# Kernel tuning notes

Measured on AMD Instinct MI355X. Metric: run time of the kernel, lower is better.

## Reference

```python
import jax, jax.numpy as jnp
from jax import lax
import numpy as np

H = 2048
LX = 32
LY = 32


def setup_inputs() -> dict:
    key = jax.random.key(0)
    ks = jax.random.split(key, 9)
    N = LX * LY
    s = 1.0 / np.sqrt(H).astype(np.float32)
    inp = {
        "x": jax.random.normal(ks[0], (N,), jnp.float32),
        # embed: Dense(1 -> H)
        "We": jax.random.normal(ks[1], (1, H), jnp.float32),
        "be": jnp.zeros((H,), jnp.float32),
        # GRUCell input gates (with bias)
        "Wir": jax.random.normal(ks[2], (H, H), jnp.float32) * s,
        "bir": jnp.zeros((H,), jnp.float32),
        "Wiz": jax.random.normal(ks[3], (H, H), jnp.float32) * s,
        "biz": jnp.zeros((H,), jnp.float32),
        "Win": jax.random.normal(ks[4], (H, H), jnp.float32) * s,
        "bin_": jnp.zeros((H,), jnp.float32),
        # GRUCell recurrent gates (hr/hz bias-free, hn with bias, as in flax)
        "Whr": jax.random.normal(ks[5], (H, H), jnp.float32) * s,
        "Whz": jax.random.normal(ks[6], (H, H), jnp.float32) * s,
        "Whn": jax.random.normal(ks[7], (H, H), jnp.float32) * s,
        "bhn": jnp.zeros((H,), jnp.float32),
        "Lx": LX,
        "Ly": LY,
    }
    return inp


def snake_order(Lx: int, Ly: int):
    idx = np.arange(Lx * Ly).reshape(Ly, Lx)
    idx[1::2] = idx[1::2, ::-1]  # reverse odd rows -> snake pattern
    return jnp.asarray(idx.reshape(-1))


def reference(x, We, be, Wir, bir, Wiz, biz, Win, bin_, Whr, Whz, Whn, bhn, Lx, Ly):
    order = snake_order(Lx, Ly)                      # (N,) visit order
    # embed each scalar site value: Dense(1->H), vectorized over all sites
    xe = x[order][:, None] * We[0][None, :] + be     # (N, H)
    # precompute input-gate projections for all steps (same math, batched)
    a_r = xe @ Wir + bir                             # (N, H)
    a_z = xe @ Wiz + biz
    a_n = xe @ Win + bin_
    h0 = jnp.zeros((Whr.shape[0],), xe.dtype)

    def step(h, g):
        ar, az, an = g
        r = jax.nn.sigmoid(ar + h @ Whr)
        z = jax.nn.sigmoid(az + h @ Whz)
        n = jnp.tanh(an + r * (h @ Whn + bhn))
        h_new = (1.0 - z) * n + z * h
        return h_new, None

    h, _ = lax.scan(step, h0, (a_r, a_z, a_n))
    return h
```

## Files before the change

### kernel.cpp

```cpp
#include <hip/hip_runtime.h>

#define HDIM 2048
#define TSTEPS 1024
#define NBLK 256
#define NTHR 512
#define CPB 8
#define TAGM 0x3FFu
#define NREP 8
#define RSTRIDE 2112u
#define SPIN_CAP (1 << 21)

typedef unsigned long long ull;

__device__ __forceinline__ int snake_src(int t) {
    int y = t >> 5, p = t & 31;
    return (y & 1) ? (y * 32 + 31 - p) : t;
}
__device__ __forceinline__ float sigmoid_f(float v) {
    return __builtin_amdgcn_rcpf(1.f + __expf(-v));
}
__device__ __forceinline__ float tanh_f(float v) {
    return 1.f - 2.f * __builtin_amdgcn_rcpf(__expf(2.f * v) + 1.f);
}
template<int G>
__device__ __forceinline__ float bcast8(float v) {
    return __uint_as_float((unsigned)__builtin_amdgcn_ds_swizzle(
        (int)__float_as_uint(v), (G << 5) | 0x18));
}

__global__ __launch_bounds__(NTHR, 1) void gru_all(
    const float* __restrict__ x,
    const float* __restrict__ We,  const float* __restrict__ be,
    const float* __restrict__ Wir, const float* __restrict__ bir,
    const float* __restrict__ Wiz, const float* __restrict__ biz,
    const float* __restrict__ Win, const float* __restrict__ bin_,
    const float* __restrict__ Whr, const float* __restrict__ Whz,
    const float* __restrict__ Whn, const float* __restrict__ bhn,
    float* __restrict__ out, unsigned* __restrict__ u0, unsigned* __restrict__ u1)
{
    const int tid  = threadIdx.x;
    const int blk  = blockIdx.x;
    const int c    = tid & 7;
    const int r    = tid >> 3;
    const int col  = blk * CPB + c;
    const int row0 = r * 32;
    const int lane = tid & 63, wv = tid >> 6;

    __shared__ float red[8][6][8];
    __shared__ float sX[TSTEPS];
    __shared__ float sAcc[3][8];
    __shared__ float sHold[8];

    for (int i = tid; i < TSTEPS; i += NTHR) sX[i] = x[snake_src(i)];

    float wr[32], wz[32], wn[32];
#pragma unroll
    for (int k = 0; k < 32; ++k) {
        size_t off = (size_t)(row0 + k) * HDIM + col;
        wr[k] = Whr[off];
        wz[k] = Whz[off];
        wn[k] = Whn[off];
    }

    float eR=0,eZ=0,eN=0,bRa=0,bZa=0,bNa=0;
#pragma unroll 8
    for (int k = 0; k < 32; ++k) {
        int row = row0 + k;
        size_t off = (size_t)row * HDIM + col;
        float we = We[row], bb = be[row];
        float w0 = Wir[off], w1 = Wiz[off], w2 = Win[off];
        eR  = fmaf(we, w0, eR);  bRa = fmaf(bb, w0, bRa);
        eZ  = fmaf(we, w1, eZ);  bZa = fmaf(bb, w1, bZa);
        eN  = fmaf(we, w2, eN);  bNa = fmaf(bb, w2, bNa);
    }
#pragma unroll
    for (int m = 8; m < 64; m <<= 1) {
        eR  += __shfl_xor(eR,  m, 64); eZ  += __shfl_xor(eZ,  m, 64);
        eN  += __shfl_xor(eN,  m, 64); bRa += __shfl_xor(bRa, m, 64);
        bZa += __shfl_xor(bZa, m, 64); bNa += __shfl_xor(bNa, m, 64);
    }
    if (lane < 8) {
        red[wv][0][lane]=eR;  red[wv][1][lane]=eZ;  red[wv][2][lane]=eN;
        red[wv][3][lane]=bRa; red[wv][4][lane]=bZa; red[wv][5][lane]=bNa;
    }
    __syncthreads();

    float vrc=0,vzc=0,vnc=0,crc=0,czc=0,cnc=0,bhc=0;
    float aN=0;
    unsigned pk1 = 0;
    if (tid < 8) {
#pragma unroll
        for (int w = 0; w < 8; ++w) {
            vrc += red[w][0][tid]; vzc += red[w][1][tid]; vnc += red[w][2][tid];
            crc += red[w][3][tid]; czc += red[w][4][tid]; cnc += red[w][5][tid];
        }
        crc += bir[col]; czc += biz[col]; cnc += bin_[col];
        bhc = bhn[col];

        float x0 = sX[0];
        float ar = fmaf(x0, vrc, crc);
        float az = fmaf(x0, vzc, czc);
        float an = fmaf(x0, vnc, cnc);
        float rg = sigmoid_f(ar), zg = sigmoid_f(az);
        float ng = tanh_f(fmaf(rg, bhc, an));
        float h1 = (1.f - zg) * ng;
        pk1 = ((__float_as_uint(h1) + 512u) & ~TAGM) | 1u;

        float x1 = sX[1];
        sAcc[0][tid] = fmaf(x1, vrc, crc);
        sAcc[1][tid] = fmaf(x1, vzc, czc);
        aN           = fmaf(x1, vnc, cnc);
        sAcc[2][tid] = bhc;
    }
    if (wv == 0) {
        unsigned pkb = __shfl(pk1, lane & 7, 64);
        __hip_atomic_store(&u1[(unsigned)(lane >> 3) * RSTRIDE + (unsigned)blk * 8u + (unsigned)(lane & 7)],
                           pkb, __ATOMIC_RELAXED, __HIP_MEMORY_SCOPE_AGENT);
    }
    __syncthreads();

    const ull  M2     = 0x000003FF000003FFull;
    const ull  repoff = (ull)(blk & 7) * (RSTRIDE / 2);
    int alive = 1;

    for (int t = 1; t < TSTEPS; ++t) {
        const unsigned* pin  = (t & 1) ? u1 : u0;
        unsigned*       pout = (t & 1) ? u0 : u1;
        const unsigned  tg   = (unsigned)t & TAGM;
        const ull       tg2  = ((ull)tg << 32) | (ull)tg;

        const ull* pp = (const ull*)pin + repoff + 2 * tid;
        ull v0 = __hip_atomic_load(&pp[0], __ATOMIC_RELAXED, __HIP_MEMORY_SCOPE_AGENT);
        ull v1 = __hip_atomic_load(&pp[1], __ATOMIC_RELAXED, __HIP_MEMORY_SCOPE_AGENT);
        if (alive) {
            int guard = 0;
            while (((v0 ^ tg2) | (v1 ^ tg2)) & M2) {
                __builtin_amdgcn_s_sleep(1);
                v0 = __hip_atomic_load(&pp[0], __ATOMIC_RELAXED, __HIP_MEMORY_SCOPE_AGENT);
                v1 = __hip_atomic_load(&pp[1], __ATOMIC_RELAXED, __HIP_MEMORY_SCOPE_AGENT);
                if (++guard > SPIN_CAP) { alive = 0; break; }
            }
        }
        float hr0 = __uint_as_float((unsigned)v0         & ~TAGM);
        float hr1 = __uint_as_float((unsigned)(v0 >> 32) & ~TAGM);
        float hr2 = __uint_as_float((unsigned)v1         & ~TAGM);
        float hr3 = __uint_as_float((unsigned)(v1 >> 32) & ~TAGM);

        if ((tid >> 1) == blk) {
            float* hs = &sHold[(tid & 1) * 4];
            hs[0] = hr0; hs[1] = hr1; hs[2] = hr2; hs[3] = hr3;
        }

        float a0 = 0.f, a1 = 0.f, a2 = 0.f;
#define GRP(G) { \
        float h0 = bcast8<G>(hr0), h1 = bcast8<G>(hr1); \
        float h2 = bcast8<G>(hr2), h3 = bcast8<G>(hr3); \
        a0 = fmaf(h0, wr[4*G+0], a0); a1 = fmaf(h0, wz[4*G+0], a1); a2 = fmaf(h0, wn[4*G+0], a2); \
        a0 = fmaf(h1, wr[4*G+1], a0); a1 = fmaf(h1, wz[4*G+1], a1); a2 = fmaf(h1, wn[4*G+1], a2); \
        a0 = fmaf(h2, wr[4*G+2], a0); a1 = fmaf(h2, wz[4*G+2], a1); a2 = fmaf(h2, wn[4*G+2], a2); \
        a0 = fmaf(h3, wr[4*G+3], a0); a1 = fmaf(h3, wz[4*G+3], a1); a2 = fmaf(h3, wn[4*G+3], a2); }
        GRP(0) GRP(1) GRP(2) GRP(3) GRP(4) GRP(5) GRP(6) GRP(7)
#undef GRP

#pragma unroll
        for (int m = 8; m < 64; m <<= 1) {
            a0 += __shfl_xor(a0, m, 64);
            a1 += __shfl_xor(a1, m, 64);
            a2 += __shfl_xor(a2, m, 64);
        }
        if (lane < 8) {
            atomicAdd(&sAcc[0][lane], a0);
            atomicAdd(&sAcc[1][lane], a1);
            atomicAdd(&sAcc[2][lane], a2);
        }
        __syncthreads();

        if (wv == 0) {
            float hnew = 0.f; unsigned pk = 0;
            if (lane < 8) {
                float Sr = sAcc[0][lane];
                float Sz = sAcc[1][lane];
                float Sn = sAcc[2][lane];
                float hold = sHold[lane];
                float rg = sigmoid_f(Sr), zg = sigmoid_f(Sz);
                float ng = tanh_f(aN + rg * Sn);
                hnew = (1.f - zg) * ng + zg * hold;
                pk = ((__float_as_uint(hnew) + 512u) & ~TAGM)
                   | ((unsigned)(t + 1) & TAGM);
            }
            if (t == TSTEPS - 1) {
                if (lane < 8) out[col] = hnew;
            } else {
                unsigned pkb = __shfl(pk, lane & 7, 64);
                __hip_atomic_store(&pout[(unsigned)(lane >> 3) * RSTRIDE + (unsigned)blk * 8u + (unsigned)(lane & 7)],
                                   pkb, __ATOMIC_RELAXED, __HIP_MEMORY_SCOPE_AGENT);
                if (lane < 8) {
                    float xn = sX[t + 1];
                    sAcc[0][lane] = fmaf(xn, vrc, crc);
                    sAcc[1][lane] = fmaf(xn, vzc, czc);
                    aN            = fmaf(xn, vnc, cnc);
                    sAcc[2][lane] = bhc;
                }
            }
        }
        __syncthreads();
    }
}

extern "C" void kernel_launch(void* const* d_in, const int* in_sizes, int n_in,
                              void* d_out, int out_size, void* d_ws, size_t ws_size,
                              hipStream_t stream) {
    const float* x    = (const float*)d_in[0];
    const float* We   = (const float*)d_in[1];
    const float* be   = (const float*)d_in[2];
    const float* Wir  = (const float*)d_in[3];
    const float* bir  = (const float*)d_in[4];
    const float* Wiz  = (const float*)d_in[5];
    const float* biz  = (const float*)d_in[6];
    const float* Win  = (const float*)d_in[7];
    const float* bin_ = (const float*)d_in[8];
    const float* Whr  = (const float*)d_in[9];
    const float* Whz  = (const float*)d_in[10];
    const float* Whn  = (const float*)d_in[11];
    const float* bhn  = (const float*)d_in[12];

    unsigned* u0 = (unsigned*)d_ws;
    unsigned* u1 = u0 + NREP * RSTRIDE;

    gru_all<<<NBLK, NTHR, 0, stream>>>(x, We, be, Wir, bir, Wiz, biz, Win, bin_,
                                       Whr, Whz, Whn, bhn,
                                       (float*)d_out, u0, u1);
}
```

Measured before the change: 2.336 ms.

## Prefetch next-step hidden state speculatively and use local h for own columns

Result: faster. 2.273 ms (-2.7%).

```diff
diff --git a/kernel.cpp b/kernel.cpp
--- a/kernel.cpp
+++ b/kernel.cpp
@@ -27,6 +27,9 @@
     return __uint_as_float((unsigned)__builtin_amdgcn_ds_swizzle(
         (int)__float_as_uint(v), (G << 5) | 0x18));
 }
+
+#define BAR_RAW() do { asm volatile("s_waitcnt lgkmcnt(0)" ::: "memory"); \
+                       __builtin_amdgcn_s_barrier(); } while (0)
 
 __global__ __launch_bounds__(NTHR, 1) void gru_all(
     const float* __restrict__ x,
@@ -49,7 +52,7 @@
     __shared__ float red[8][6][8];
     __shared__ float sX[TSTEPS];
     __shared__ float sAcc[3][8];
-    __shared__ float sHold[8];
+    __shared__ float sNext[8];
 
     for (int i = tid; i < TSTEPS; i += NTHR) sX[i] = x[snake_src(i)];
 
@@ -105,6 +108,7 @@
         float ng = tanh_f(fmaf(rg, bhc, an));
         float h1 = (1.f - zg) * ng;
         pk1 = ((__float_as_uint(h1) + 512u) & ~TAGM) | 1u;
+        sNext[tid] = h1;
 
         float x1 = sX[1];
         sAcc[0][tid] = fmaf(x1, vrc, crc);
@@ -121,7 +125,15 @@
 
     const ull  M2     = 0x000003FF000003FFull;
     const ull  repoff = (ull)(blk & 7) * (RSTRIDE / 2);
+    const bool selfcol = ((tid >> 1) == blk);
     int alive = 1;
+
+    ull v0p, v1p;
+    {
+        const ull* pp1 = (const ull*)u1 + repoff + 2 * tid;
+        v0p = __hip_atomic_load(&pp1[0], __ATOMIC_RELAXED, __HIP_MEMORY_SCOPE_AGENT);
+        v1p = __hip_atomic_load(&pp1[1], __ATOMIC_RELAXED, __HIP_MEMORY_SCOPE_AGENT);
+    }
 
     for (int t = 1; t < TSTEPS; ++t) {
         const unsigned* pin  = (t & 1) ? u1 : u0;
@@ -129,26 +141,26 @@
         const unsigned  tg   = (unsigned)t & TAGM;
         const ull       tg2  = ((ull)tg << 32) | (ull)tg;
 
-        const ull* pp = (const ull*)pin + repoff + 2 * tid;
-        ull v0 = __hip_atomic_load(&pp[0], __ATOMIC_RELAXED, __HIP_MEMORY_SCOPE_AGENT);
-        ull v1 = __hip_atomic_load(&pp[1], __ATOMIC_RELAXED, __HIP_MEMORY_SCOPE_AGENT);
-        if (alive) {
-            int guard = 0;
-            while (((v0 ^ tg2) | (v1 ^ tg2)) & M2) {
-                __builtin_amdgcn_s_sleep(1);
-                v0 = __hip_atomic_load(&pp[0], __ATOMIC_RELAXED, __HIP_MEMORY_SCOPE_AGENT);
-                v1 = __hip_atomic_load(&pp[1], __ATOMIC_RELAXED, __HIP_MEMORY_SCOPE_AGENT);
-                if (++guard > SPIN_CAP) { alive = 0; break; }
+        float hr0, hr1, hr2, hr3;
+        if (selfcol) {
+            const float* sn = &sNext[(tid & 1) * 4];
+            hr0 = sn[0]; hr1 = sn[1]; hr2 = sn[2]; hr3 = sn[3];
+        } else {
+            ull v0 = v0p, v1 = v1p;
+            if ((((v0 ^ tg2) | (v1 ^ tg2)) & M2) && alive) {
+                const ull* pp = (const ull*)pin + repoff + 2 * tid;
+                int guard = 0;
+                do {
+                    __builtin_amdgcn_s_sleep(1);
+                    v0 = __hip_atomic_load(&pp[0], __ATOMIC_RELAXED, __HIP_MEMORY_SCOPE_AGENT);
+                    v1 = __hip_atomic_load(&pp[1], __ATOMIC_RELAXED, __HIP_MEMORY_SCOPE_AGENT);
+                    if (++guard > SPIN_CAP) { alive = 0; break; }
+                } while (((v0 ^ tg2) | (v1 ^ tg2)) & M2);
             }
-        }
-        float hr0 = __uint_as_float((unsigned)v0         & ~TAGM);
-        float hr1 = __uint_as_float((unsigned)(v0 >> 32) & ~TAGM);
-        float hr2 = __uint_as_float((unsigned)v1         & ~TAGM);
-        float hr3 = __uint_as_float((unsigned)(v1 >> 32) & ~TAGM);
-
-        if ((tid >> 1) == blk) {
-            float* hs = &sHold[(tid & 1) * 4];
-            hs[0] = hr0; hs[1] = hr1; hs[2] = hr2; hs[3] = hr3;
+            hr0 = __uint_as_float((unsigned)v0         & ~TAGM);
+            hr1 = __uint_as_float((unsigned)(v0 >> 32) & ~TAGM);
+            hr2 = __uint_as_float((unsigned)v1         & ~TAGM);
+            hr3 = __uint_as_float((unsigned)(v1 >> 32) & ~TAGM);
         }
 
         float a0 = 0.f, a1 = 0.f, a2 = 0.f;
@@ -173,7 +185,13 @@
             atomicAdd(&sAcc[1][lane], a1);
             atomicAdd(&sAcc[2][lane], a2);
         }
-        __syncthreads();
+
+        {
+            const ull* ppn = (const ull*)pout + repoff + 2 * tid;
+            v0p = __hip_atomic_load(&ppn[0], __ATOMIC_RELAXED, __HIP_MEMORY_SCOPE_AGENT);
+            v1p = __hip_atomic_load(&ppn[1], __ATOMIC_RELAXED, __HIP_MEMORY_SCOPE_AGENT);
+        }
+        BAR_RAW();
 
         if (wv == 0) {
             float hnew = 0.f; unsigned pk = 0;
@@ -181,7 +199,7 @@
                 float Sr = sAcc[0][lane];
                 float Sz = sAcc[1][lane];
                 float Sn = sAcc[2][lane];
-                float hold = sHold[lane];
+                float hold = sNext[lane];
                 float rg = sigmoid_f(Sr), zg = sigmoid_f(Sz);
                 float ng = tanh_f(aN + rg * Sn);
                 hnew = (1.f - zg) * ng + zg * hold;
@@ -195,6 +213,7 @@
                 __hip_atomic_store(&pout[(unsigned)(lane >> 3) * RSTRIDE + (unsigned)blk * 8u + (unsigned)(lane & 7)],
                                    pkb, __ATOMIC_RELAXED, __HIP_MEMORY_SCOPE_AGENT);
                 if (lane < 8) {
+                    sNext[lane] = hnew;
                     float xn = sX[t + 1];
                     sAcc[0][lane] = fmaf(xn, vrc, crc);
                     sAcc[1][lane] = fmaf(xn, vzc, czc);
@@ -203,7 +222,7 @@
                 }
             }
         }
-        __syncthreads();
+        BAR_RAW();
     }
 }
 
```
